# Optimization experiments

Measured on AMD Instinct MI355X. Metric: run time of the kernel, lower is better.

Reference implementation:

```python
import jax, jax.numpy as jnp
import numpy as np

B, S, D, H = 2, 2048, 1024, 16
DH = D // H  # dim_per_head = 64


def setup_inputs() -> dict:
    key = jax.random.key(0)
    ks = jax.random.split(key, 12)
    scale = 1.0 / np.sqrt(D)
    inp = {
        "key": jax.random.normal(ks[0], (B, S, D), jnp.float32),
        "value": jax.random.normal(ks[1], (B, S, D), jnp.float32),
        "query": jax.random.normal(ks[2], (B, S, D), jnp.float32),
        "mask": jax.random.randint(ks[3], (B, S, S), 0, 2) == 1,
        "Wq": jax.random.normal(ks[4], (D, D), jnp.float32) * scale,
        "bq": jnp.zeros((D,), jnp.float32),
        "Wk": jax.random.normal(ks[5], (D, D), jnp.float32) * scale,
        "bk": jnp.zeros((D,), jnp.float32),
        "Wv": jax.random.normal(ks[6], (D, D), jnp.float32) * scale,
        "bv": jnp.zeros((D,), jnp.float32),
        "Wo": jax.random.normal(ks[7], (D, D), jnp.float32) * scale,
        "bo": jnp.zeros((D,), jnp.float32),
    }
    return inp


def reference(key, value, query, mask, Wq, bq, Wk, bk, Wv, bv, Wo, bo):
    b, s, d = query.shape
    dh = d // H

    def split_heads(x):  # [b, s, d] -> [b, H, s, dh]
        return x.reshape(b, -1, H, dh).transpose(0, 2, 1, 3)

    q = split_heads(query @ Wq + bq) / jnp.sqrt(jnp.float32(dh))
    k = split_heads(key @ Wk + bk)
    v = split_heads(value @ Wv + bv)

    scores = jnp.einsum("bhqd,bhkd->bhqk", q, k)  # [b, H, s, s]
    scores = jnp.where(mask[:, None, :, :], jnp.float32(-1e18), scores)
    attn = jax.nn.softmax(scores, axis=-1)  # dropout is identity in eval
    ctx = jnp.einsum("bhqk,bhkd->bhqd", attn, v)
    ctx = ctx.transpose(0, 2, 1, 3).reshape(b, s, d)
    return ctx @ Wo + bo
```

## Files before the change

### kernel.cpp

```cpp
#include <hip/hip_runtime.h>
#include <hip/hip_bf16.h>

#define BATCH  2
#define SEQ    2048
#define DMODEL 1024
#define NHEAD  16
#define DHEAD  64
#define NTOK   (BATCH * SEQ)

using f32x4 = __attribute__((ext_vector_type(4))) float;
using s16x4 = __attribute__((ext_vector_type(4))) short;
using s16x8 = __attribute__((ext_vector_type(8))) short;

__device__ __forceinline__ short f2bf(float f) {
  __hip_bfloat16 h = __float2bfloat16(f);
  return *(short*)&h;
}

__device__ __forceinline__ void gload_lds16(const short* g, short* l) {
  __builtin_amdgcn_global_load_lds(
      (const __attribute__((address_space(1))) void*)g,
      (__attribute__((address_space(3))) void*)l, 16, 0, 0);
}

__global__ __launch_bounds__(256) void wtrans_kernel(
    const float* __restrict__ Wq, const float* __restrict__ Wk,
    const float* __restrict__ Wv, const float* __restrict__ Wo,
    short* __restrict__ Wt) {
  __shared__ short tile[64][72];
  const float* W = blockIdx.z == 0 ? Wq : blockIdx.z == 1 ? Wk
                 : blockIdx.z == 2 ? Wv : Wo;
  short* out = Wt + (size_t)blockIdx.z * DMODEL * DMODEL;
  int k0 = blockIdx.x * 64, n0 = blockIdx.y * 64;
  int t = threadIdx.x;
#pragma unroll
  for (int i = 0; i < 4; ++i) {
    int idx = t + i * 256;
    int row = idx >> 4, c4 = idx & 15;
    f32x4 v = *(const f32x4*)(W + (size_t)(k0 + row) * DMODEL + n0 + c4 * 4);
    s16x4 p;
    p[0] = f2bf(v[0]); p[1] = f2bf(v[1]); p[2] = f2bf(v[2]); p[3] = f2bf(v[3]);
    *(s16x4*)&tile[row][c4 * 4] = p;
  }
  __syncthreads();
#pragma unroll
  for (int i = 0; i < 2; ++i) {
    int idx = t + i * 256;
    int nrow = idx >> 3, c8 = idx & 7;
    s16x8 p;
#pragma unroll
    for (int j = 0; j < 8; ++j) p[j] = tile[c8 * 8 + j][nrow];
    *(s16x8*)(out + (size_t)(n0 + nrow) * DMODEL + k0 + c8 * 8) = p;
  }
}

__global__ __launch_bounds__(256) void mpack_kernel(
    const int* __restrict__ mask, unsigned long long* __restrict__ Mp) {
  const int total_words = BATCH * SEQ * (SEQ / 64);
  int lane = threadIdx.x & 63;
  int wv = blockIdx.x * 4 + (threadIdx.x >> 6);
  int nw = gridDim.x * 4;
  for (int w = wv; w < total_words; w += nw) {
    int mv = mask[(size_t)w * 64 + lane];
    unsigned long long bits = __ballot(mv != 0);
    if (lane == 0) Mp[w] = bits;
  }
}

__global__ __launch_bounds__(256) void proj_qkv_kernel(
    const float* __restrict__ Xq, const float* __restrict__ Xk,
    const float* __restrict__ Xv, const short* __restrict__ Wt,
    const float* __restrict__ bq, const float* __restrict__ bk,
    const float* __restrict__ bv, short* __restrict__ QKV) {
  __shared__ short As[128][32];
  __shared__ short Bs[128][32];
  const int sel = blockIdx.z;
  const float* X    = sel == 0 ? Xq : sel == 1 ? Xk : Xv;
  const float* bias = sel == 0 ? bq : sel == 1 ? bk : bv;
  const short* Wsel = Wt + (size_t)sel * DMODEL * DMODEL;
  short* Obuf = QKV + (size_t)sel * ((size_t)BATCH * NHEAD * SEQ * DHEAD);
  const float scale = sel == 0 ? 0.18033688011111793f : 1.0f;

  int m0 = blockIdx.x * 128, n0 = blockIdx.y * 128;
  int t = threadIdx.x, wid = t >> 6, lane = t & 63;
  int lr = lane & 15, lg = lane >> 4;
  int wr = wid >> 1, wc = wid & 1;
  f32x4 acc[4][4] = {};

  for (int kt = 0; kt < DMODEL / 32; ++kt) {
    int k0 = kt * 32;
    __syncthreads();
#pragma unroll
    for (int i = 0; i < 2; ++i) {
      int c = i * 256 + t;
      short* lbase = &Bs[0][0] + (size_t)((i * 256 + (t & ~63)) << 3);
      gload_lds16(Wsel + (size_t)(n0 + (c >> 2)) * DMODEL + k0 + ((c & 3) << 3),
                  lbase);
    }
#pragma unroll
    for (int i = 0; i < 2; ++i) {
      int idx = t + i * 256, row = idx >> 2, c8 = idx & 3;
      const float* src = X + (size_t)(m0 + row) * DMODEL + k0 + c8 * 8;
      f32x4 v0 = *(const f32x4*)src;
      f32x4 v1 = *(const f32x4*)(src + 4);
      s16x8 p;
      p[0] = f2bf(v0[0]); p[1] = f2bf(v0[1]); p[2] = f2bf(v0[2]); p[3] = f2bf(v0[3]);
      p[4] = f2bf(v1[0]); p[5] = f2bf(v1[1]); p[6] = f2bf(v1[2]); p[7] = f2bf(v1[3]);
      *(s16x8*)&As[row][c8 * 8] = p;
    }
    __syncthreads();
    s16x8 afr[4], bfr[4];
#pragma unroll
    for (int mi = 0; mi < 4; ++mi)
      afr[mi] = *(const s16x8*)&As[wr * 64 + mi * 16 + lr][lg * 8];
#pragma unroll
    for (int ni = 0; ni < 4; ++ni)
      bfr[ni] = *(const s16x8*)&Bs[wc * 64 + ni * 16 + lr][lg * 8];
#pragma unroll
    for (int mi = 0; mi < 4; ++mi)
#pragma unroll
      for (int ni = 0; ni < 4; ++ni)
        acc[mi][ni] = __builtin_amdgcn_mfma_f32_16x16x32_bf16(
            afr[mi], bfr[ni], acc[mi][ni], 0, 0, 0);
  }
  if (sel == 2) {
    int bq_ = m0 >> 11;
    int s0 = (m0 & (SEQ - 1)) + wr * 64 + lg * 4;
#pragma unroll
    for (int mi = 0; mi < 4; ++mi)
#pragma unroll
      for (int ni = 0; ni < 4; ++ni) {
        int n = n0 + wc * 64 + ni * 16 + lr;
        float bv_ = bias[n];
        int h = n >> 6, d = n & 63;
        s16x4 pk;
#pragma unroll
        for (int r = 0; r < 4; ++r) pk[r] = f2bf(acc[mi][ni][r] + bv_);
        *(s16x4*)&Obuf[((size_t)(bq_ * NHEAD + h) * DHEAD + d) * SEQ
                       + s0 + mi * 16] = pk;
      }
  } else {
#pragma unroll
    for (int mi = 0; mi < 4; ++mi)
#pragma unroll
      for (int ni = 0; ni < 4; ++ni) {
        int n = n0 + wc * 64 + ni * 16 + lr;
        float bv_ = bias[n];
        int h = n >> 6, d = n & 63;
#pragma unroll
        for (int r = 0; r < 4; ++r) {
          int m = m0 + wr * 64 + mi * 16 + lg * 4 + r;
          int b = m >> 11, s = m & (SEQ - 1);
          float val = (acc[mi][ni][r] + bv_) * scale;
          Obuf[((size_t)(b * NHEAD + h) * SEQ + s) * DHEAD + d] = f2bf(val);
        }
      }
  }
}

__global__ __launch_bounds__(256) void attn_kernel(
    const short* __restrict__ Qb, const short* __restrict__ Kb,
    const short* __restrict__ VbT, const unsigned long long* __restrict__ Mp,
    short* __restrict__ Ctx) {
  __shared__ short Ks[2][64 * 64];
  __shared__ short Vt[2][64 * 64];
  __shared__ short Ps[4 * 16 * 64];
  int qt = blockIdx.x, bh = blockIdx.y;
  int b = bh >> 4, h = bh & 15;
  int q0 = qt * 64;
  int t = threadIdx.x, wid = t >> 6, lane = t & 63;
  int lr = lane & 15, lg = lane >> 4;
  int lr7 = lr & 7;

  const short* Qrow = Qb + ((size_t)bh * SEQ + q0 + wid * 16 + lr) * DHEAD;
  s16x8 qf[2];
  qf[0] = *(const s16x8*)(Qrow + lg * 8);
  qf[1] = *(const s16x8*)(Qrow + 32 + lg * 8);

  const short* KbB = Kb + (size_t)bh * SEQ * DHEAD;
  const short* VtB = VbT + (size_t)bh * DHEAD * SEQ;

  const int srow = lane >> 3;
  const int schunk = ((lane & 7) ^ srow) * 8;

  float m_run = -1e30f, l_run = 0.f;
  f32x4 o_acc[4] = {};

  const unsigned long long* mrow =
      Mp + ((size_t)b * SEQ + q0 + wid * 16 + lr) * (SEQ / 64);

#define STAGE(bufi, k0s)                                                      \
  {                                                                           \
    _Pragma("unroll")                                                         \
    for (int i = 0; i < 2; ++i) {                                             \
      int rbase = wid * 16 + i * 8;                                           \
      gload_lds16(KbB + (size_t)((k0s) + rbase + srow) * DHEAD + schunk,      \
                  &Ks[bufi][rbase * 64]);                                     \
      gload_lds16(VtB + (size_t)(rbase + srow) * SEQ + (k0s) + schunk,        \
                  &Vt[bufi][rbase * 64]);                                     \
    }                                                                         \
  }

  unsigned long long mw_cur = mrow[0];
  STAGE(0, 0);
  asm volatile("s_waitcnt vmcnt(0)" ::: "memory");
  __syncthreads();

  int cur = 0;
  for (int kt = 0; kt < SEQ / 64; ++kt) {
    unsigned long long mw_next = 0;
    if (kt + 1 < SEQ / 64) {
      STAGE(cur ^ 1, (kt + 1) * 64);
      mw_next = mrow[kt + 1];
    }
    const short* KsC = Ks[cur];
    const short* VtC = Vt[cur];

    f32x4 sfr[4];
    __builtin_amdgcn_s_setprio(1);
#pragma unroll
    for (int nf = 0; nf < 4; ++nf) {
      int row = nf * 16 + lr;
      s16x8 kf0 = *(const s16x8*)&KsC[row * 64 + ((lg ^ lr7) << 3)];
      s16x8 kf1 = *(const s16x8*)&KsC[row * 64 + (((4 + lg) ^ lr7) << 3)];
      f32x4 c = {};
      c = __builtin_amdgcn_mfma_f32_16x16x32_bf16(kf0, qf[0], c, 0, 0, 0);
      c = __builtin_amdgcn_mfma_f32_16x16x32_bf16(kf1, qf[1], c, 0, 0, 0);
      sfr[nf] = c;
    }
    __builtin_amdgcn_s_setprio(0);

    unsigned w0 = (unsigned)(mw_cur >> (lg * 4));
    unsigned w1 = (unsigned)(mw_cur >> (lg * 4 + 32));
#pragma unroll
    for (int nf = 0; nf < 4; ++nf)
#pragma unroll
      for (int r = 0; r < 4; ++r) {
        unsigned bit = (nf < 2) ? (w0 >> (nf * 16 + r)) : (w1 >> ((nf - 2) * 16 + r));
        if (bit & 1u) sfr[nf][r] = -1e30f;
      }
    float tm = fmaxf(fmaxf(fmaxf(sfr[0][0], sfr[0][1]), fmaxf(sfr[0][2], sfr[0][3])),
                     fmaxf(fmaxf(sfr[1][0], sfr[1][1]), fmaxf(sfr[1][2], sfr[1][3])));
    float tm2 = fmaxf(fmaxf(fmaxf(sfr[2][0], sfr[2][1]), fmaxf(sfr[2][2], sfr[2][3])),
                      fmaxf(fmaxf(sfr[3][0], sfr[3][1]), fmaxf(sfr[3][2], sfr[3][3])));
    tm = fmaxf(tm, tm2);
    tm = fmaxf(tm, __shfl_xor(tm, 16, 64));
    tm = fmaxf(tm, __shfl_xor(tm, 32, 64));

    bool small = __all(tm <= m_run + 8.0f);
    if (!small) {
      float mnew = fmaxf(m_run, tm);
      float scl = __builtin_amdgcn_exp2f(m_run - mnew);
      m_run = mnew;
      l_run *= scl;
      float scl_o[4];
#pragma unroll
      for (int r = 0; r < 4; ++r) scl_o[r] = __shfl(scl, lg * 4 + r, 64);
#pragma unroll
      for (int nf = 0; nf < 4; ++nf)
#pragma unroll
        for (int r = 0; r < 4; ++r) o_acc[nf][r] *= scl_o[r];
    }
    float ps4[4];
#pragma unroll
    for (int nf = 0; nf < 4; ++nf) {
#pragma unroll
      for (int r = 0; r < 4; ++r)
        sfr[nf][r] = __builtin_amdgcn_exp2f(sfr[nf][r] - m_run);
      ps4[nf] = (sfr[nf][0] + sfr[nf][1]) + (sfr[nf][2] + sfr[nf][3]);
    }
    float ps = (ps4[0] + ps4[1]) + (ps4[2] + ps4[3]);
    ps += __shfl_xor(ps, 16, 64);
    ps += __shfl_xor(ps, 32, 64);
    l_run += ps;

    int psbase = wid * (16 * 64) + lr * 64;
#pragma unroll
    for (int nf = 0; nf < 4; ++nf) {
      s16x4 pk;
#pragma unroll
      for (int r = 0; r < 4; ++r) pk[r] = f2bf(sfr[nf][r]);
      *(s16x4*)&Ps[psbase + ((((2 * nf + (lg >> 1)) ^ lr7) << 3) | ((lg & 1) << 2))] = pk;
    }
    asm volatile("s_waitcnt lgkmcnt(0)" ::: "memory");
    __builtin_amdgcn_sched_barrier(0);

    __builtin_amdgcn_s_setprio(1);
#pragma unroll
    for (int ks = 0; ks < 2; ++ks) {
      s16x8 pf = *(const s16x8*)&Ps[psbase + (((ks * 4 + lg) ^ lr7) << 3)];
#pragma unroll
      for (int nf = 0; nf < 4; ++nf) {
        int d = nf * 16 + lr;
        s16x8 vf = *(const s16x8*)&VtC[d * 64 + (((ks * 4 + lg) ^ lr7) << 3)];
        o_acc[nf] = __builtin_amdgcn_mfma_f32_16x16x32_bf16(pf, vf, o_acc[nf], 0, 0, 0);
      }
    }
    __builtin_amdgcn_s_setprio(0);

    asm volatile("s_waitcnt vmcnt(0)" ::: "memory");
    __syncthreads();
    cur ^= 1;
    mw_cur = mw_next;
  }
#undef STAGE
  float l_o[4];
#pragma unroll
  for (int r = 0; r < 4; ++r) l_o[r] = __shfl(l_run, lg * 4 + r, 64);
#pragma unroll
  for (int nf = 0; nf < 4; ++nf)
#pragma unroll
    for (int r = 0; r < 4; ++r) {
      int srow_ = q0 + wid * 16 + lg * 4 + r;
      float val = o_acc[nf][r] / l_o[r];
      Ctx[((size_t)b * SEQ + srow_) * DMODEL + h * DHEAD + nf * 16 + lr] = f2bf(val);
    }
}

__global__ __launch_bounds__(256) void proj_out_kernel(
    const short* __restrict__ Ctx, const short* __restrict__ Wot,
    const float* __restrict__ bo, float* __restrict__ Out) {
  __shared__ short As[128][32];
  __shared__ short Bs[128][32];
  int m0 = blockIdx.x * 128, n0 = blockIdx.y * 128;
  int t = threadIdx.x, wid = t >> 6, lane = t & 63;
  int lr = lane & 15, lg = lane >> 4;
  int wr = wid >> 1, wc = wid & 1;
  f32x4 acc[4][4] = {};

  for (int kt = 0; kt < DMODEL / 32; ++kt) {
    int k0 = kt * 32;
    __syncthreads();
#pragma unroll
    for (int i = 0; i < 2; ++i) {
      int c = i * 256 + t;
      size_t lofs = (size_t)((i * 256 + (t & ~63)) << 3);
      gload_lds16(Ctx + (size_t)(m0 + (c >> 2)) * DMODEL + k0 + ((c & 3) << 3),
                  &As[0][0] + lofs);
      gload_lds16(Wot + (size_t)(n0 + (c >> 2)) * DMODEL + k0 + ((c & 3) << 3),
                  &Bs[0][0] + lofs);
    }
    __syncthreads();
    s16x8 afr[4], bfr[4];
#pragma unroll
    for (int mi = 0; mi < 4; ++mi)
      afr[mi] = *(const s16x8*)&As[wr * 64 + mi * 16 + lr][lg * 8];
#pragma unroll
    for (int ni = 0; ni < 4; ++ni)
      bfr[ni] = *(const s16x8*)&Bs[wc * 64 + ni * 16 + lr][lg * 8];
#pragma unroll
    for (int mi = 0; mi < 4; ++mi)
#pragma unroll
      for (int ni = 0; ni < 4; ++ni)
        acc[mi][ni] = __builtin_amdgcn_mfma_f32_16x16x32_bf16(
            afr[mi], bfr[ni], acc[mi][ni], 0, 0, 0);
  }
#pragma unroll
  for (int mi = 0; mi < 4; ++mi)
#pragma unroll
    for (int ni = 0; ni < 4; ++ni) {
      int n = n0 + wc * 64 + ni * 16 + lr;
      float bv_ = bo[n];
#pragma unroll
      for (int r = 0; r < 4; ++r) {
        int m = m0 + wr * 64 + mi * 16 + lg * 4 + r;
        Out[(size_t)m * DMODEL + n] = acc[mi][ni][r] + bv_;
      }
    }
}

extern "C" void kernel_launch(void* const* d_in, const int* in_sizes, int n_in,
                              void* d_out, int out_size, void* d_ws, size_t ws_size,
                              hipStream_t stream) {
  const float* key_in   = (const float*)d_in[0];
  const float* value_in = (const float*)d_in[1];
  const float* query_in = (const float*)d_in[2];
  const int*   mask     = (const int*)d_in[3];
  const float* Wq = (const float*)d_in[4];
  const float* bq = (const float*)d_in[5];
  const float* Wk = (const float*)d_in[6];
  const float* bk = (const float*)d_in[7];
  const float* Wv = (const float*)d_in[8];
  const float* bv = (const float*)d_in[9];
  const float* Wo = (const float*)d_in[10];
  const float* bo = (const float*)d_in[11];
  float* out = (float*)d_out;

  short* ws = (short*)d_ws;
  const size_t WSZ   = (size_t)DMODEL * DMODEL;
  const size_t QKVSZ = (size_t)BATCH * NHEAD * SEQ * DHEAD;
  short* Wt  = ws;
  short* QKV = ws + 4 * WSZ;
  short* Qb  = QKV;
  short* Kb  = QKV + QKVSZ;
  short* VbT = QKV + 2 * QKVSZ;
  short* Ctx = QKV + 3 * QKVSZ;
  unsigned long long* Mp = (unsigned long long*)ws;

  wtrans_kernel<<<dim3(16, 16, 4), 256, 0, stream>>>(Wq, Wk, Wv, Wo, Wt);
  proj_qkv_kernel<<<dim3(32, 8, 3), 256, 0, stream>>>(
      query_in, key_in, value_in, Wt, bq, bk, bv, QKV);
  mpack_kernel<<<dim3(1024), 256, 0, stream>>>(mask, Mp);
  attn_kernel<<<dim3(32, 32), 256, 0, stream>>>(Qb, Kb, VbT, Mp, Ctx);
  proj_out_kernel<<<dim3(32, 8), 256, 0, stream>>>(Ctx, Wt + 3 * WSZ, bo, out);
}
```

Measured before the change: 185.1 us.

## Double-buffer LDS tiles in QKV and output projection GEMMs

Both projection GEMM kernels now use two LDS buffers per operand. The next K-tile's global loads, and for QKV the fp32 activation prefetch into registers, are issued before the MFMA block on the current tile, so each iteration needs one barrier instead of two. Wave priority is raised around the MFMA sequence. This costs double the shared memory per block and extra registers for the prefetched activations, which may lower occupancy.

```diff
diff --git a/kernel.cpp b/kernel.cpp
--- a/kernel.cpp
+++ b/kernel.cpp
@@ -72,8 +72,8 @@
     const float* __restrict__ Xv, const short* __restrict__ Wt,
     const float* __restrict__ bq, const float* __restrict__ bk,
     const float* __restrict__ bv, short* __restrict__ QKV) {
-  __shared__ short As[128][32];
-  __shared__ short Bs[128][32];
+  __shared__ short As[2][128 * 32];
+  __shared__ short Bs[2][128 * 32];
   const int sel = blockIdx.z;
   const float* X    = sel == 0 ? Xq : sel == 1 ? Xk : Xv;
   const float* bias = sel == 0 ? bq : sel == 1 ? bk : bv;
@@ -87,42 +87,64 @@
   int wr = wid >> 1, wc = wid & 1;
   f32x4 acc[4][4] = {};
 
+  const int ar0 = t >> 2, ac0 = (t & 3) << 3;
+  const float* Arow0 = X + (size_t)(m0 + ar0) * DMODEL + ac0;
+  const float* Arow1 = Arow0 + (size_t)64 * DMODEL;
+  const int aofs0 = ar0 * 32 + ac0, aofs1 = aofs0 + 64 * 32;
+  const short* Brow0 = Wsel + (size_t)(n0 + ar0) * DMODEL + ac0;
+  const short* Brow1 = Brow0 + (size_t)64 * DMODEL;
+  const int bofs0 = (t & ~63) << 3, bofs1 = bofs0 + 256 * 8;
+
+  f32x4 a00, a01, a10, a11;
+#define LOADA(k0s) {                                                          \
+    a00 = *(const f32x4*)(Arow0 + (k0s));                                     \
+    a01 = *(const f32x4*)(Arow0 + (k0s) + 4);                                 \
+    a10 = *(const f32x4*)(Arow1 + (k0s));                                     \
+    a11 = *(const f32x4*)(Arow1 + (k0s) + 4); }
+#define STAGEB(bufi, k0s) {                                                   \
+    gload_lds16(Brow0 + (k0s), &Bs[bufi][0] + bofs0);                         \
+    gload_lds16(Brow1 + (k0s), &Bs[bufi][0] + bofs1); }
+#define WRITEA(bufi) {                                                        \
+    s16x8 p0, p1;                                                             \
+    p0[0]=f2bf(a00[0]); p0[1]=f2bf(a00[1]); p0[2]=f2bf(a00[2]); p0[3]=f2bf(a00[3]); \
+    p0[4]=f2bf(a01[0]); p0[5]=f2bf(a01[1]); p0[6]=f2bf(a01[2]); p0[7]=f2bf(a01[3]); \
+    p1[0]=f2bf(a10[0]); p1[1]=f2bf(a10[1]); p1[2]=f2bf(a10[2]); p1[3]=f2bf(a10[3]); \
+    p1[4]=f2bf(a11[0]); p1[5]=f2bf(a11[1]); p1[6]=f2bf(a11[2]); p1[7]=f2bf(a11[3]); \
+    *(s16x8*)(&As[bufi][0] + aofs0) = p0;                                     \
+    *(s16x8*)(&As[bufi][0] + aofs1) = p1; }
+
+  LOADA(0); STAGEB(0, 0); WRITEA(0);
+  __syncthreads();
+
+  int cur = 0;
   for (int kt = 0; kt < DMODEL / 32; ++kt) {
-    int k0 = kt * 32;
-    __syncthreads();
-#pragma unroll
-    for (int i = 0; i < 2; ++i) {
-      int c = i * 256 + t;
-      short* lbase = &Bs[0][0] + (size_t)((i * 256 + (t & ~63)) << 3);
-      gload_lds16(Wsel + (size_t)(n0 + (c >> 2)) * DMODEL + k0 + ((c & 3) << 3),
-                  lbase);
-    }
-#pragma unroll
-    for (int i = 0; i < 2; ++i) {
-      int idx = t + i * 256, row = idx >> 2, c8 = idx & 3;
-      const float* src = X + (size_t)(m0 + row) * DMODEL + k0 + c8 * 8;
-      f32x4 v0 = *(const f32x4*)src;
-      f32x4 v1 = *(const f32x4*)(src + 4);
-      s16x8 p;
-      p[0] = f2bf(v0[0]); p[1] = f2bf(v0[1]); p[2] = f2bf(v0[2]); p[3] = f2bf(v0[3]);
-      p[4] = f2bf(v1[0]); p[5] = f2bf(v1[1]); p[6] = f2bf(v1[2]); p[7] = f2bf(v1[3]);
-      *(s16x8*)&As[row][c8 * 8] = p;
-    }
-    __syncthreads();
+    if (kt + 1 < DMODEL / 32) {
+      LOADA((kt + 1) * 32);
+      STAGEB(cur ^ 1, (kt + 1) * 32);
+    }
     s16x8 afr[4], bfr[4];
 #pragma unroll
     for (int mi = 0; mi < 4; ++mi)
-      afr[mi] = *(const s16x8*)&As[wr * 64 + mi * 16 + lr][lg * 8];
+      afr[mi] = *(const s16x8*)(&As[cur][0] + (wr * 64 + mi * 16 + lr) * 32 + lg * 8);
 #pragma unroll
     for (int ni = 0; ni < 4; ++ni)
-      bfr[ni] = *(const s16x8*)&Bs[wc * 64 + ni * 16 + lr][lg * 8];
+      bfr[ni] = *(const s16x8*)(&Bs[cur][0] + (wc * 64 + ni * 16 + lr) * 32 + lg * 8);
+    __builtin_amdgcn_s_setprio(1);
 #pragma unroll
     for (int mi = 0; mi < 4; ++mi)
 #pragma unroll
       for (int ni = 0; ni < 4; ++ni)
         acc[mi][ni] = __builtin_amdgcn_mfma_f32_16x16x32_bf16(
             afr[mi], bfr[ni], acc[mi][ni], 0, 0, 0);
-  }
+    __builtin_amdgcn_s_setprio(0);
+    if (kt + 1 < DMODEL / 32) WRITEA(cur ^ 1);
+    __syncthreads();
+    cur ^= 1;
+  }
+#undef LOADA
+#undef STAGEB
+#undef WRITEA
+
   if (sel == 2) {
     int bq_ = m0 >> 11;
     int s0 = (m0 & (SEQ - 1)) + wr * 64 + lg * 4;
@@ -320,41 +342,53 @@
 __global__ __launch_bounds__(256) void proj_out_kernel(
     const short* __restrict__ Ctx, const short* __restrict__ Wot,
     const float* __restrict__ bo, float* __restrict__ Out) {
-  __shared__ short As[128][32];
-  __shared__ short Bs[128][32];
+  __shared__ short As[2][128 * 32];
+  __shared__ short Bs[2][128 * 32];
   int m0 = blockIdx.x * 128, n0 = blockIdx.y * 128;
   int t = threadIdx.x, wid = t >> 6, lane = t & 63;
   int lr = lane & 15, lg = lane >> 4;
   int wr = wid >> 1, wc = wid & 1;
   f32x4 acc[4][4] = {};
 
+  const int gr0 = t >> 2, gc0 = (t & 3) << 3;
+  const short* Actx0 = Ctx + (size_t)(m0 + gr0) * DMODEL + gc0;
+  const short* Actx1 = Actx0 + (size_t)64 * DMODEL;
+  const short* Bwo0 = Wot + (size_t)(n0 + gr0) * DMODEL + gc0;
+  const short* Bwo1 = Bwo0 + (size_t)64 * DMODEL;
+  const int lofs0 = (t & ~63) << 3, lofs1 = lofs0 + 256 * 8;
+
+#define STAGE_PO(bufi, k0s) {                                                 \
+    gload_lds16(Actx0 + (k0s), &As[bufi][0] + lofs0);                         \
+    gload_lds16(Actx1 + (k0s), &As[bufi][0] + lofs1);                         \
+    gload_lds16(Bwo0 + (k0s), &Bs[bufi][0] + lofs0);                          \
+    gload_lds16(Bwo1 + (k0s), &Bs[bufi][0] + lofs1); }
+
+  STAGE_PO(0, 0);
+  __syncthreads();
+
+  int cur = 0;
   for (int kt = 0; kt < DMODEL / 32; ++kt) {
-    int k0 = kt * 32;
-    __syncthreads();
-#pragma unroll
-    for (int i = 0; i < 2; ++i) {
-      int c = i * 256 + t;
-      size_t lofs = (size_t)((i * 256 + (t & ~63)) << 3);
-      gload_lds16(Ctx + (size_t)(m0 + (c >> 2)) * DMODEL + k0 + ((c & 3) << 3),
-                  &As[0][0] + lofs);
-      gload_lds16(Wot + (size_t)(n0 + (c >> 2)) * DMODEL + k0 + ((c & 3) << 3),
-                  &Bs[0][0] + lofs);
-    }
-    __syncthreads();
+    if (kt + 1 < DMODEL / 32) STAGE_PO(cur ^ 1, (kt + 1) * 32);
     s16x8 afr[4], bfr[4];
 #pragma unroll
     for (int mi = 0; mi < 4; ++mi)
-      afr[mi] = *(const s16x8*)&As[wr * 64 + mi * 16 + lr][lg * 8];
+      afr[mi] = *(const s16x8*)(&As[cur][0] + (wr * 64 + mi * 16 + lr) * 32 + lg * 8);
 #pragma unroll
     for (int ni = 0; ni < 4; ++ni)
-      bfr[ni] = *(const s16x8*)&Bs[wc * 64 + ni * 16 + lr][lg * 8];
+      bfr[ni] = *(const s16x8*)(&Bs[cur][0] + (wc * 64 + ni * 16 + lr) * 32 + lg * 8);
+    __builtin_amdgcn_s_setprio(1);
 #pragma unroll
     for (int mi = 0; mi < 4; ++mi)
 #pragma unroll
       for (int ni = 0; ni < 4; ++ni)
         acc[mi][ni] = __builtin_amdgcn_mfma_f32_16x16x32_bf16(
             afr[mi], bfr[ni], acc[mi][ni], 0, 0, 0);
-  }
+    __builtin_amdgcn_s_setprio(0);
+    __syncthreads();
+    cur ^= 1;
+  }
+#undef STAGE_PO
+
 #pragma unroll
   for (int mi = 0; mi < 4; ++mi)
 #pragma unroll
```

Result: slower. 190.5 us (+2.9%).
